# Kernel optimization log

Hardware: AMD Instinct MI355X
Metric: run time of the kernel (lower is better)

Reference implementation:

```python
import jax, jax.numpy as jnp
import numpy as np

OS_FACTOR = 1.5
DELAY = 1                      # int(floor(os_factor))
K = DELAY / OS_FACTOR          # 1 / (os_factor / delay)
B, T, I, H = 64, 16384, 1, 64


def setup_inputs() -> dict:
    key = jax.random.key(0)
    k1, k2, k3, k4, k5 = jax.random.split(key, 5)
    s = 1.0 / np.sqrt(H).astype(np.float32)  # torch RNNCell init range
    return {
        "x": jax.random.normal(k1, (B, T, I), dtype=jnp.float32),
        "W_ih": jax.random.uniform(k2, (H, I), minval=-s, maxval=s, dtype=jnp.float32),
        "W_hh": jax.random.uniform(k3, (H, H), minval=-s, maxval=s, dtype=jnp.float32),
        "b_ih": jax.random.uniform(k4, (H,), minval=-s, maxval=s, dtype=jnp.float32),
        "b_hh": jax.random.uniform(k5, (H,), minval=-s, maxval=s, dtype=jnp.float32),
    }


def reference(x, W_ih, W_hh, b_ih, b_hh):
    # Precompute the input projection for all timesteps (parallel part).
    xw = jnp.einsum("bti,hi->bth", x, W_ih) + b_ih  # [B, T, H]

    def step(h_prev, xw_t):
        # torch.nn.RNNCell(tanh): h_next = tanh(W_ih x + b_ih + W_hh h + b_hh)
        cell = jnp.tanh(xw_t + h_prev @ W_hh.T + b_hh)
        # delay-line read (delay=1 -> previous state) + fractional blend
        h = h_prev + K * (cell - h_prev)
        return h, h

    h0 = jnp.zeros((x.shape[0], W_hh.shape[0]), dtype=x.dtype)  # zero-init delay line
    h_last, states_t = jax.lax.scan(step, h0, jnp.swapaxes(xw, 0, 1))  # scan over T
    states = jnp.swapaxes(states_t, 0, 1)  # [B, T, H]
    return states, h_last[None]  # (states, h.view(1, B, H))
```

## Files before the change

kernel.cpp:

```cpp
#include <hip/hip_runtime.h>

#define T_LEN 16384
#define HDIM 64
#define BATCH 64

#define KBLEND      (2.0f / 3.0f)
#define ONE_MINUS_K (1.0f / 3.0f)
#define KK          (KBLEND * ONE_MINUS_K)

#define C2    2.8853900817779268f
#define C2K   (C2 * KBLEND)
#define C2KK  (C2 * KK)

typedef _Float16 f16x8 __attribute__((ext_vector_type(8)));
typedef float    f32x4 __attribute__((ext_vector_type(4)));

__device__ __forceinline__ float lane_bcast(float v, int lane) {
    return __int_as_float(__builtin_amdgcn_readlane(__float_as_int(v), lane));
}

__global__ __launch_bounds__(HDIM)
__attribute__((amdgpu_waves_per_eu(1, 1)))
void rnn_delayline_kernel(
    const float* __restrict__ x,
    const float* __restrict__ Wih,
    const float* __restrict__ Whh,
    const float* __restrict__ bih,
    const float* __restrict__ bhh,
    float* __restrict__ out_states,
    float* __restrict__ out_hlast)
{
    const int lane = threadIdx.x;
    const int b    = blockIdx.x;

    __shared__ __align__(16) _Float16 hbuf[HDIM];

    const float* xb = x + (size_t)b * T_LEN;

    f16x8 Bf[8];
    {
        const int n = lane & 15, g = lane >> 4;
        #pragma unroll
        for (int j = 0; j < 4; ++j) {
            const float* wrow = Whh + (j * 16 + n) * HDIM;
            #pragma unroll
            for (int s = 0; s < 2; ++s) {
                const float4* wp = reinterpret_cast<const float4*>(wrow + s * 32 + g * 8);
                float4 v0 = wp[0], v1 = wp[1];
                Bf[j*2+s] = (f16x8){(_Float16)v0.x, (_Float16)v0.y,
                                    (_Float16)v0.z, (_Float16)v0.w,
                                    (_Float16)v1.x, (_Float16)v1.y,
                                    (_Float16)v1.z, (_Float16)v1.w};
            }
        }
    }

    const float wihC2  = C2 * Wih[lane];
    const float biasC2 = C2 * (bih[lane] + bhh[lane]);

    const char* hbB = reinterpret_cast<const char*>(hbuf);
    const int   gofs = (lane >> 4) * 16;

    const bool selLo = ((lane >> 4) & 1) != 0;
    const bool selHi = ((lane >> 4) & 2) != 0;

    float h = 0.0f, dot = 0.0f, G = 0.0f;

    float xcur = xb[lane];
    float* outp = out_states + (size_t)b * T_LEN * HDIM + lane;

    const int NCHUNK = T_LEN / HDIM;
    for (int c = 0; c < NCHUNK; ++c) {
        float xnext = 0.0f;
        if (c + 1 < NCHUNK) xnext = xb[(size_t)(c + 1) * HDIM + lane];

        #pragma unroll 4
        for (int tt = 0; tt < HDIM; ++tt) {
            asm volatile("" : "+v"(Bf[0]), "+v"(Bf[1]), "+v"(Bf[2]), "+v"(Bf[3]),
                              "+v"(Bf[4]), "+v"(Bf[5]), "+v"(Bf[6]), "+v"(Bf[7]));

            float xt = lane_bcast(xcur, tt);
            float cb = fmaf(xt, wihC2, biasC2) + G;

            float targ = fmaf(C2K, dot, cb);
            float e    = __builtin_amdgcn_exp2f(targ);
            float r    = __builtin_amdgcn_rcpf(1.0f + e);
            float cell = fmaf(-2.0f, r, 1.0f);

            hbuf[lane] = (_Float16)cell;

            G = fmaf(ONE_MINUS_K, G, C2KK * dot);
            h = fmaf(KBLEND, cell - h, h);
            *outp = h;
            outp += HDIM;

            f16x8 a0 = *reinterpret_cast<const f16x8*>(hbB + gofs);
            f16x8 a1 = *reinterpret_cast<const f16x8*>(hbB + 64 + gofs);

            f32x4 d0 = __builtin_amdgcn_mfma_f32_16x16x32_f16(a0, Bf[0], (f32x4){0,0,0,0}, 0, 0, 0);
            f32x4 d1 = __builtin_amdgcn_mfma_f32_16x16x32_f16(a0, Bf[2], (f32x4){0,0,0,0}, 0, 0, 0);
            f32x4 d2 = __builtin_amdgcn_mfma_f32_16x16x32_f16(a0, Bf[4], (f32x4){0,0,0,0}, 0, 0, 0);
            f32x4 d3 = __builtin_amdgcn_mfma_f32_16x16x32_f16(a0, Bf[6], (f32x4){0,0,0,0}, 0, 0, 0);
            d0 = __builtin_amdgcn_mfma_f32_16x16x32_f16(a1, Bf[1], d0, 0, 0, 0);
            d1 = __builtin_amdgcn_mfma_f32_16x16x32_f16(a1, Bf[3], d1, 0, 0, 0);
            d2 = __builtin_amdgcn_mfma_f32_16x16x32_f16(a1, Bf[5], d2, 0, 0, 0);
            d3 = __builtin_amdgcn_mfma_f32_16x16x32_f16(a1, Bf[7], d3, 0, 0, 0);

            float t01 = selLo ? d1[0] : d0[0];
            float t23 = selLo ? d3[0] : d2[0];
            dot = selHi ? t23 : t01;
        }

        xcur = xnext;
    }

    out_hlast[b * HDIM + lane] = h;
}

extern "C" void kernel_launch(void* const* d_in, const int* in_sizes, int n_in,
                              void* d_out, int out_size, void* d_ws, size_t ws_size,
                              hipStream_t stream) {
    const float* x   = (const float*)d_in[0];
    const float* Wih = (const float*)d_in[1];
    const float* Whh = (const float*)d_in[2];
    const float* bih = (const float*)d_in[3];
    const float* bhh = (const float*)d_in[4];

    float* out_states = (float*)d_out;
    float* out_hlast  = out_states + (size_t)BATCH * T_LEN * HDIM;

    rnn_delayline_kernel<<<dim3(BATCH), dim3(HDIM), 0, stream>>>(
        x, Wih, Whh, bih, bhh, out_states, out_hlast);
}
```

Before: 2.398 ms.

## Split recurrence and output blending/stores into producer and consumer waves

The block now runs two waves. One wave runs the tanh/MFMA recurrence and writes each step's cell into a two-chunk LDS ring, then publishes a per-chunk flag. The second wave polls that flag, reads the cells back, applies the blend to form h and issues all global state stores. This takes the blend and the global stores off the serial recurrence path. In exchange, h is now blended from the f16-rounded cell rather than the fp32 one. There is also no back-pressure, so the producer can overwrite a ring slot before the consumer has read it.

Measured after the change: 2.331 ms, median of 2. 1.03x faster.

```diff
diff --git a/kernel.cpp b/kernel.cpp
--- a/kernel.cpp
+++ b/kernel.cpp
@@ -3,6 +3,7 @@
 #define T_LEN 16384
 #define HDIM 64
 #define BATCH 64
+#define RING  128
 
 #define KBLEND      (2.0f / 3.0f)
 #define ONE_MINUS_K (1.0f / 3.0f)
@@ -19,7 +20,7 @@
     return __int_as_float(__builtin_amdgcn_readlane(__float_as_int(v), lane));
 }
 
-__global__ __launch_bounds__(HDIM)
+__global__ __launch_bounds__(2 * HDIM)
 __attribute__((amdgpu_waves_per_eu(1, 1)))
 void rnn_delayline_kernel(
     const float* __restrict__ x,
@@ -30,91 +31,113 @@
     float* __restrict__ out_states,
     float* __restrict__ out_hlast)
 {
-    const int lane = threadIdx.x;
+    const int tid  = threadIdx.x;
+    const int lane = tid & (HDIM - 1);
     const int b    = blockIdx.x;
 
-    __shared__ __align__(16) _Float16 hbuf[HDIM];
+    __shared__ __align__(16) _Float16 ring[RING][HDIM];
+    __shared__ int flag;
+
+    if (tid == 0) flag = 0;
+    __syncthreads();
 
     const float* xb = x + (size_t)b * T_LEN;
+    const int NCHUNK = T_LEN / HDIM;
 
-    f16x8 Bf[8];
-    {
-        const int n = lane & 15, g = lane >> 4;
-        #pragma unroll
-        for (int j = 0; j < 4; ++j) {
-            const float* wrow = Whh + (j * 16 + n) * HDIM;
+    if (tid < HDIM) {
+        f16x8 Bf[8];
+        {
+            const int n = lane & 15, g = lane >> 4;
             #pragma unroll
-            for (int s = 0; s < 2; ++s) {
-                const float4* wp = reinterpret_cast<const float4*>(wrow + s * 32 + g * 8);
-                float4 v0 = wp[0], v1 = wp[1];
-                Bf[j*2+s] = (f16x8){(_Float16)v0.x, (_Float16)v0.y,
-                                    (_Float16)v0.z, (_Float16)v0.w,
-                                    (_Float16)v1.x, (_Float16)v1.y,
-                                    (_Float16)v1.z, (_Float16)v1.w};
+            for (int j = 0; j < 4; ++j) {
+                const float* wrow = Whh + (j * 16 + n) * HDIM;
+                #pragma unroll
+                for (int s = 0; s < 2; ++s) {
+                    const float4* wp = reinterpret_cast<const float4*>(wrow + s * 32 + g * 8);
+                    float4 v0 = wp[0], v1 = wp[1];
+                    Bf[j*2+s] = (f16x8){(_Float16)v0.x, (_Float16)v0.y,
+                                        (_Float16)v0.z, (_Float16)v0.w,
+                                        (_Float16)v1.x, (_Float16)v1.y,
+                                        (_Float16)v1.z, (_Float16)v1.w};
+                }
             }
         }
+
+        const float wihC2  = C2 * Wih[lane];
+        const float biasC2 = C2 * (bih[lane] + bhh[lane]);
+
+        const int  g8    = (lane >> 4) * 8;
+        const bool selLo = ((lane >> 4) & 1) != 0;
+        const bool selHi = ((lane >> 4) & 2) != 0;
+
+        float dot = 0.0f, G = 0.0f;
+        float xcur = xb[lane];
+
+        for (int c = 0; c < NCHUNK; ++c) {
+            float xnext = 0.0f;
+            if (c + 1 < NCHUNK) xnext = xb[(size_t)(c + 1) * HDIM + lane];
+            const int sbase = (c & 1) * 64;
+
+            #pragma unroll 4
+            for (int tt = 0; tt < HDIM; ++tt) {
+                asm volatile("" : "+v"(Bf[0]), "+v"(Bf[1]), "+v"(Bf[2]), "+v"(Bf[3]),
+                                  "+v"(Bf[4]), "+v"(Bf[5]), "+v"(Bf[6]), "+v"(Bf[7]));
+
+                float xt = lane_bcast(xcur, tt);
+                float cb = fmaf(xt, wihC2, biasC2) + G;
+
+                float targ = fmaf(C2K, dot, cb);
+                float e    = __builtin_amdgcn_exp2f(targ);
+                float r    = __builtin_amdgcn_rcpf(1.0f + e);
+                float cell = fmaf(-2.0f, r, 1.0f);
+
+                const int slot = sbase + tt;
+                ring[slot][lane] = (_Float16)cell;
+
+                G = fmaf(ONE_MINUS_K, G, C2KK * dot);
+
+                f16x8 a0 = *reinterpret_cast<const f16x8*>(&ring[slot][g8]);
+                f16x8 a1 = *reinterpret_cast<const f16x8*>(&ring[slot][32 + g8]);
+
+                f32x4 d0 = __builtin_amdgcn_mfma_f32_16x16x32_f16(a0, Bf[0], (f32x4){0,0,0,0}, 0, 0, 0);
+                f32x4 d1 = __builtin_amdgcn_mfma_f32_16x16x32_f16(a0, Bf[2], (f32x4){0,0,0,0}, 0, 0, 0);
+                f32x4 d2 = __builtin_amdgcn_mfma_f32_16x16x32_f16(a0, Bf[4], (f32x4){0,0,0,0}, 0, 0, 0);
+                f32x4 d3 = __builtin_amdgcn_mfma_f32_16x16x32_f16(a0, Bf[6], (f32x4){0,0,0,0}, 0, 0, 0);
+                d0 = __builtin_amdgcn_mfma_f32_16x16x32_f16(a1, Bf[1], d0, 0, 0, 0);
+                d1 = __builtin_amdgcn_mfma_f32_16x16x32_f16(a1, Bf[3], d1, 0, 0, 0);
+                d2 = __builtin_amdgcn_mfma_f32_16x16x32_f16(a1, Bf[5], d2, 0, 0, 0);
+                d3 = __builtin_amdgcn_mfma_f32_16x16x32_f16(a1, Bf[7], d3, 0, 0, 0);
+
+                float t01 = selLo ? d1[0] : d0[0];
+                float t23 = selLo ? d3[0] : d2[0];
+                dot = selHi ? t23 : t01;
+            }
+
+            xcur = xnext;
+            if (lane == 0)
+                __hip_atomic_store(&flag, c + 1, __ATOMIC_RELEASE,
+                                   __HIP_MEMORY_SCOPE_WORKGROUP);
+        }
+    } else {
+        float h = 0.0f;
+        float* outp = out_states + (size_t)b * T_LEN * HDIM + lane;
+
+        for (int c = 0; c < NCHUNK; ++c) {
+            while (__hip_atomic_load(&flag, __ATOMIC_ACQUIRE,
+                                     __HIP_MEMORY_SCOPE_WORKGROUP) <= c) {
+                __builtin_amdgcn_s_sleep(2);
+            }
+            const int sbase = (c & 1) * 64;
+            #pragma unroll 4
+            for (int tt = 0; tt < HDIM; ++tt) {
+                float cell = (float)ring[sbase + tt][lane];
+                h = fmaf(KBLEND, cell - h, h);
+                *outp = h;
+                outp += HDIM;
+            }
+        }
+        out_hlast[b * HDIM + lane] = h;
     }
-
-    const float wihC2  = C2 * Wih[lane];
-    const float biasC2 = C2 * (bih[lane] + bhh[lane]);
-
-    const char* hbB = reinterpret_cast<const char*>(hbuf);
-    const int   gofs = (lane >> 4) * 16;
-
-    const bool selLo = ((lane >> 4) & 1) != 0;
-    const bool selHi = ((lane >> 4) & 2) != 0;
-
-    float h = 0.0f, dot = 0.0f, G = 0.0f;
-
-    float xcur = xb[lane];
-    float* outp = out_states + (size_t)b * T_LEN * HDIM + lane;
-
-    const int NCHUNK = T_LEN / HDIM;
-    for (int c = 0; c < NCHUNK; ++c) {
-        float xnext = 0.0f;
-        if (c + 1 < NCHUNK) xnext = xb[(size_t)(c + 1) * HDIM + lane];
-
-        #pragma unroll 4
-        for (int tt = 0; tt < HDIM; ++tt) {
-            asm volatile("" : "+v"(Bf[0]), "+v"(Bf[1]), "+v"(Bf[2]), "+v"(Bf[3]),
-                              "+v"(Bf[4]), "+v"(Bf[5]), "+v"(Bf[6]), "+v"(Bf[7]));
-
-            float xt = lane_bcast(xcur, tt);
-            float cb = fmaf(xt, wihC2, biasC2) + G;
-
-            float targ = fmaf(C2K, dot, cb);
-            float e    = __builtin_amdgcn_exp2f(targ);
-            float r    = __builtin_amdgcn_rcpf(1.0f + e);
-            float cell = fmaf(-2.0f, r, 1.0f);
-
-            hbuf[lane] = (_Float16)cell;
-
-            G = fmaf(ONE_MINUS_K, G, C2KK * dot);
-            h = fmaf(KBLEND, cell - h, h);
-            *outp = h;
-            outp += HDIM;
-
-            f16x8 a0 = *reinterpret_cast<const f16x8*>(hbB + gofs);
-            f16x8 a1 = *reinterpret_cast<const f16x8*>(hbB + 64 + gofs);
-
-            f32x4 d0 = __builtin_amdgcn_mfma_f32_16x16x32_f16(a0, Bf[0], (f32x4){0,0,0,0}, 0, 0, 0);
-            f32x4 d1 = __builtin_amdgcn_mfma_f32_16x16x32_f16(a0, Bf[2], (f32x4){0,0,0,0}, 0, 0, 0);
-            f32x4 d2 = __builtin_amdgcn_mfma_f32_16x16x32_f16(a0, Bf[4], (f32x4){0,0,0,0}, 0, 0, 0);
-            f32x4 d3 = __builtin_amdgcn_mfma_f32_16x16x32_f16(a0, Bf[6], (f32x4){0,0,0,0}, 0, 0, 0);
-            d0 = __builtin_amdgcn_mfma_f32_16x16x32_f16(a1, Bf[1], d0, 0, 0, 0);
-            d1 = __builtin_amdgcn_mfma_f32_16x16x32_f16(a1, Bf[3], d1, 0, 0, 0);
-            d2 = __builtin_amdgcn_mfma_f32_16x16x32_f16(a1, Bf[5], d2, 0, 0, 0);
-            d3 = __builtin_amdgcn_mfma_f32_16x16x32_f16(a1, Bf[7], d3, 0, 0, 0);
-
-            float t01 = selLo ? d1[0] : d0[0];
-            float t23 = selLo ? d3[0] : d2[0];
-            dot = selHi ? t23 : t01;
-        }
-
-        xcur = xnext;
-    }
-
-    out_hlast[b * HDIM + lane] = h;
 }
 
 extern "C" void kernel_launch(void* const* d_in, const int* in_sizes, int n_in,
@@ -129,6 +152,6 @@
     float* out_states = (float*)d_out;
     float* out_hlast  = out_states + (size_t)BATCH * T_LEN * HDIM;
 
-    rnn_delayline_kernel<<<dim3(BATCH), dim3(HDIM), 0, stream>>>(
+    rnn_delayline_kernel<<<dim3(BATCH), dim3(2 * HDIM), 0, stream>>>(
         x, Wih, Whh, bih, bhh, out_states, out_hlast);
 }
```
